# Kernel optimization log

Measured on AMD Instinct MI355X. Metric: run time of the kernel, lower is better.

Reference implementation:

```python
import jax, jax.numpy as jnp
import numpy as np

H = 1024


def setup_inputs() -> dict:
    key = jax.random.key(0)
    ks = jax.random.split(key, 7)
    x = jax.random.normal(ks[0], (8, 2048, H), dtype=jnp.float32)
    s = 1.0 / np.sqrt(H)
    Wq = jax.random.normal(ks[1], (H, H), dtype=jnp.float32) * s
    bq = jnp.zeros((H,), dtype=jnp.float32)
    Wk = jax.random.normal(ks[2], (H, H), dtype=jnp.float32) * s
    bk = jnp.zeros((H,), dtype=jnp.float32)
    Wv = jax.random.normal(ks[3], (H, H), dtype=jnp.float32) * s
    bv = jnp.zeros((H,), dtype=jnp.float32)
    return {"x": x, "Wq": Wq, "bq": bq, "Wk": Wk, "bk": bk, "Wv": Wv, "bv": bv}


def reference(x, Wq, bq, Wk, bk, Wv, bv):
    # q,k,v: [B,S,H]
    q = jnp.einsum('bsh,hd->bsd', x, Wq) + bq
    k = jnp.einsum('bsh,hd->bsd', x, Wk) + bk
    v = jnp.einsum('bsh,hd->bsd', x, Wv) + bv
    scale = 1.0 / jnp.sqrt(jnp.asarray(x.shape[-1], dtype=x.dtype))
    scores = jnp.einsum('bqd,bkd->bqk', q, k) * scale  # [B,S,S]
    attn = jax.nn.softmax(scores, axis=-1)
    return jnp.einsum('bqk,bkd->bqd', attn, v)
```

## Files before the change

### kernel.cpp

```cpp
#include <hip/hip_runtime.h>

typedef _Float16 half8  __attribute__((ext_vector_type(8)));
typedef _Float16 half4v __attribute__((ext_vector_type(4)));
typedef float    floatx4 __attribute__((ext_vector_type(4)));

#define GLD_LDS16(g, l)                                                        \
  __builtin_amdgcn_global_load_lds(                                            \
      (const __attribute__((address_space(1))) void*)(g),                      \
      (__attribute__((address_space(3))) void*)(l), 16, 0, 0)

template <int EPI>
__global__ __launch_bounds__(256) void gemm_bt(
    const _Float16* __restrict__ A, const _Float16* __restrict__ B,
    void* __restrict__ Cv, void* __restrict__ Cv2, int lda, int ldb, int ldc,
    int kdim, long long sAz, long long sBz, long long sCz,
    const float* __restrict__ b0, const float* __restrict__ b1,
    const float* __restrict__ b2, float* __restrict__ rowsum, float scale) {
  __shared__ _Float16 sA[128 * 64];
  __shared__ _Float16 sB[128 * 64];

  const int bid = blockIdx.x;
  int z, m0, n0;
  if (EPI == 0) {
    const int xcd = bid & 7, j = bid >> 3;
    z = j >> 7;
    m0 = (xcd * 16 + ((j >> 3) & 15)) * 128;
    n0 = (j & 7) * 128;
  } else if (EPI == 2) {
    z = bid & 7;
    const int j = bid >> 3;
    m0 = (j >> 4) * 128;
    n0 = (j & 15) * 128;
  } else {
    z = bid & 7;
    const int j = bid >> 3;
    m0 = (j >> 3) * 128;
    n0 = (j & 7) * 128;
  }

  A += (size_t)z * sAz;
  B += (size_t)z * sBz;

  const int tid = threadIdx.x;
  const int wid = tid >> 6;
  const int lane = tid & 63;

  const int wm = (wid & 1) * 64;
  const int wn = (wid >> 1) * 64;
  const int lr = lane & 15;
  const int lk = lane >> 4;

  floatx4 acc[4][4];
#pragma unroll
  for (int i = 0; i < 4; ++i)
#pragma unroll
    for (int j = 0; j < 4; ++j)
#pragma unroll
      for (int r = 0; r < 4; ++r) acc[i][j][r] = 0.f;

  const _Float16* gA[4];
  const _Float16* gB[4];
  int ub[4];
#pragma unroll
  for (int j = 0; j < 4; ++j) {
    const int s = j * 256 + wid * 64 + lane;
    const int row = s >> 3;
    const int kc = (s & 7) ^ (row & 7);
    gA[j] = A + (size_t)(m0 + row) * lda + kc * 8;
    gB[j] = B + (size_t)(n0 + row) * ldb + kc * 8;
    ub[j] = (j * 256 + wid * 64) * 8;
  }

  for (int k0 = 0; k0 < kdim; k0 += 64) {
#pragma unroll
    for (int j = 0; j < 4; ++j) {
      GLD_LDS16(gA[j], &sA[ub[j]]);
      GLD_LDS16(gB[j], &sB[ub[j]]);
      gA[j] += 64;
      gB[j] += 64;
    }
    __syncthreads();

#pragma unroll
    for (int ks = 0; ks < 2; ++ks) {
      half8 af[4], bf[4];
#pragma unroll
      for (int t = 0; t < 4; ++t) {
        const int kcl = ks * 4 + lk;
        const int ra = wm + t * 16 + lr;
        af[t] = *(const half8*)&sA[(ra * 8 + (kcl ^ (ra & 7))) * 8];
        const int rb = wn + t * 16 + lr;
        bf[t] = *(const half8*)&sB[(rb * 8 + (kcl ^ (rb & 7))) * 8];
      }
#pragma unroll
      for (int mt = 0; mt < 4; ++mt)
#pragma unroll
        for (int nt = 0; nt < 4; ++nt)
          acc[mt][nt] = __builtin_amdgcn_mfma_f32_16x16x32_f16(
              af[mt], bf[nt], acc[mt][nt], 0, 0, 0);
    }
    __syncthreads();
  }

  if (EPI == 0) {
    const float* bias = (z == 0) ? b0 : ((z == 1) ? b1 : b2);
#pragma unroll
    for (int mt = 0; mt < 4; ++mt) {
#pragma unroll
      for (int nt = 0; nt < 4; ++nt) {
#pragma unroll
        for (int r = 0; r < 4; ++r) {
          const int gm = m0 + wm + mt * 16 + lk * 4 + r;
          const int gn = n0 + wn + nt * 16 + lr;
          const float v = acc[mt][nt][r] + bias[gn];
          if (z < 2) {
            ((_Float16*)Cv)[(size_t)z * 16777216 + (size_t)gm * 1024 + gn] =
                (_Float16)v;
          } else {
            const int b = gm >> 11, sseq = gm & 2047;
            ((_Float16*)Cv2)[(size_t)b * 2097152 + (size_t)gn * 2048 + sseq] =
                (_Float16)v;
          }
        }
      }
    }
  } else if (EPI == 2) {
    const float c1 = scale * 1.44269504f;
    const float c0 = -5.77078016f;
    _Float16* Sout = (_Float16*)Cv + (size_t)z * sCz;
    float* rs = rowsum + z * 2048;
#pragma unroll
    for (int mt = 0; mt < 4; ++mt) {
#pragma unroll
      for (int r = 0; r < 4; ++r) {
        const int gm = m0 + wm + mt * 16 + lk * 4 + r;
        float part = 0.f;
#pragma unroll
        for (int nt = 0; nt < 4; ++nt) {
          const int gn = n0 + wn + nt * 16 + lr;
          const float p = exp2f(fmaf(acc[mt][nt][r], c1, c0));
          const _Float16 ph = (_Float16)p;
          Sout[(size_t)gm * ldc + gn] = ph;
          part += (float)ph;
        }
#pragma unroll
        for (int o = 1; o < 16; o <<= 1) part += __shfl_xor(part, o);
        if (lr == 0) atomicAdd(&rs[gm], part);
      }
    }
  } else {
    float* O = (float*)Cv + (size_t)z * sCz;
    const float* rs = rowsum + z * 2048;
#pragma unroll
    for (int mt = 0; mt < 4; ++mt) {
#pragma unroll
      for (int r = 0; r < 4; ++r) {
        const int gm = m0 + wm + mt * 16 + lk * 4 + r;
        const float inv = 1.0f / rs[gm];
#pragma unroll
        for (int nt = 0; nt < 4; ++nt) {
          const int gn = n0 + wn + nt * 16 + lr;
          O[(size_t)gm * ldc + gn] = acc[mt][nt][r] * inv;
        }
      }
    }
  }
}

__global__ __launch_bounds__(256) void prep(
    const float* __restrict__ x, _Float16* __restrict__ xb,
    const float* __restrict__ W0, const float* __restrict__ W1,
    const float* __restrict__ W2, _Float16* __restrict__ Wt) {
  const int bid = blockIdx.x;
  const int tid = threadIdx.x;
  if (bid < 16384) {
    const int i = bid * 256 + tid;
    const float4 v = ((const float4*)x)[i];
    half4v h;
    h[0] = (_Float16)v.x;
    h[1] = (_Float16)v.y;
    h[2] = (_Float16)v.z;
    h[3] = (_Float16)v.w;
    ((half4v*)xb)[i] = h;
    return;
  }
  __shared__ float tile[32][33];
  const int q = bid - 16384;
  const int bz = q >> 10;
  const int t = q & 1023;
  const int d0 = (t & 31) * 32, h0 = (t >> 5) * 32;
  const float* W = bz == 0 ? W0 : (bz == 1 ? W1 : W2);
  _Float16* T = Wt + (size_t)bz * 1048576;
  const int tx = tid & 31, ty = tid >> 5;
#pragma unroll
  for (int i = 0; i < 4; ++i)
    tile[ty + i * 8][tx] = W[(size_t)(h0 + ty + i * 8) * 1024 + d0 + tx];
  __syncthreads();
#pragma unroll
  for (int i = 0; i < 4; ++i)
    T[(size_t)(d0 + ty + i * 8) * 1024 + h0 + tx] =
        (_Float16)tile[tx][ty + i * 8];
}

extern "C" void kernel_launch(void* const* d_in, const int* in_sizes, int n_in,
                              void* d_out, int out_size, void* d_ws,
                              size_t ws_size, hipStream_t stream) {
  const float* x = (const float*)d_in[0];
  const float* Wq = (const float*)d_in[1];
  const float* bq = (const float*)d_in[2];
  const float* Wk = (const float*)d_in[3];
  const float* bk = (const float*)d_in[4];
  const float* Wv = (const float*)d_in[5];
  const float* bv = (const float*)d_in[6];
  float* out = (float*)d_out;

  char* w = (char*)d_ws;
  _Float16* xb = (_Float16*)(w);
  _Float16* Wt = (_Float16*)(w + 33554432);
  _Float16* QK = (_Float16*)(w + 39845888);
  _Float16* Vt = (_Float16*)(w + 106954752);
  _Float16* S  = (_Float16*)(w + 140509184);
  float* rowsum = (float*)(w);

  prep<<<19456, 256, 0, stream>>>(x, xb, Wq, Wk, Wv, Wt);
  gemm_bt<0><<<3072, 256, 0, stream>>>(
      xb, Wt, QK, Vt, 1024, 1024, 1024, 1024, 0LL, 1048576LL, 0LL, bq, bk, bv,
      nullptr, 1.f);
  hipMemsetAsync(rowsum, 0, 8 * 2048 * sizeof(float), stream);
  gemm_bt<2><<<2048, 256, 0, stream>>>(
      QK, QK + 16777216, S, nullptr, 1024, 1024, 2048, 1024, 2097152LL,
      2097152LL, 4194304LL, nullptr, nullptr, nullptr, rowsum, 0.03125f);
  gemm_bt<3><<<1024, 256, 0, stream>>>(
      S, Vt, out, nullptr, 2048, 2048, 1024, 2048, 4194304LL, 2097152LL,
      2097152LL, nullptr, nullptr, nullptr, rowsum, 1.f);

  (void)in_sizes;
  (void)n_in;
  (void)out_size;
  (void)ws_size;
}
```

Baseline: 479.7 us.

## Use 256x256 tiles with 8 waves and double-buffered LDS ping-pong pipeline

Grows the GEMM tile from 128x128 to 256x256 and the block from 256 to 512 threads. The K loop becomes double-buffered in 128 KB of LDS, with global-to-LDS prefetch of the next K tile interleaved between MFMA phases using explicit vmcnt waits, barriers and setprio. The aim is to hide global load latency, raise data reuse per tile and improve MFMA utilisation. In exchange it uses more registers and LDS, and grid sizes drop (256 blocks for the final GEMM), which may underfill the 256 CUs.

```diff
diff --git a/kernel.cpp b/kernel.cpp
--- a/kernel.cpp
+++ b/kernel.cpp
@@ -9,33 +9,133 @@
       (const __attribute__((address_space(1))) void*)(g),                      \
       (__attribute__((address_space(3))) void*)(l), 16, 0, 0)
 
+#define SBAR() __builtin_amdgcn_s_barrier()
+#define WAITVM2() asm volatile("s_waitcnt vmcnt(2)" ::: "memory")
+#define WAITVM0() asm volatile("s_waitcnt vmcnt(0)" ::: "memory")
+#define SCHED0() __builtin_amdgcn_sched_barrier(0)
+
+
+#define STG_A(c, ht, ko)                                                       \
+  do {                                                                         \
+    GLD_LDS16(A0 + (size_t)(ht) * lda128 + (ko),                               \
+              &lds[(c) * 32768 + ((ht) * 1024 + wid * 128) * 8]);              \
+    GLD_LDS16(A1 + (size_t)(ht) * lda128 + (ko),                               \
+              &lds[(c) * 32768 + ((ht) * 1024 + wid * 128 + 64) * 8]);         \
+  } while (0)
+#define STG_B(c, ht, ko)                                                       \
+  do {                                                                         \
+    GLD_LDS16(B0 + (size_t)(ht) * ldb128 + (ko),                               \
+              &lds[(c) * 32768 + 16384 + ((ht) * 1024 + wid * 128) * 8]);      \
+    GLD_LDS16(B1 + (size_t)(ht) * ldb128 + (ko),                               \
+              &lds[(c) * 32768 + 16384 + ((ht) * 1024 + wid * 128 + 64) * 8]); \
+  } while (0)
+
+#define RDA(dst, c, mt, ks)                                                    \
+  do {                                                                         \
+    const int ra_ = wm + (mt) * 16 + lr;                                       \
+    dst = *(const half8*)&lds[(c) * 32768 +                                    \
+                              (ra_ * 8 + (((ks) * 4 + lk) ^ (ra_ & 7))) * 8];  \
+  } while (0)
+#define RDB(dst, c, nt, ks)                                                    \
+  do {                                                                         \
+    const int rb_ = wn + (nt) * 16 + lr;                                       \
+    dst = *(const half8*)&lds[(c) * 32768 + 16384 +                            \
+                              (rb_ * 8 + (((ks) * 4 + lk) ^ (rb_ & 7))) * 8];  \
+  } while (0)
+
+#define MM4x2(MB, NB, BF)                                                      \
+  do {                                                                         \
+    _Pragma("unroll") for (int mt_ = 0; mt_ < 4; ++mt_)                        \
+        _Pragma("unroll") for (int n_ = 0; n_ < 2; ++n_)                       \
+            _Pragma("unroll") for (int ks_ = 0; ks_ < 2; ++ks_)                \
+                acc[(MB) + mt_][(NB) + n_] =                                   \
+        __builtin_amdgcn_mfma_f32_16x16x32_f16(                                \
+            af[mt_][ks_], BF[n_][ks_], acc[(MB) + mt_][(NB) + n_], 0, 0, 0);   \
+  } while (0)
+
+#define KBLOCK(CUR, KT)                                                        \
+  do {                                                                         \
+    const int ko_ = ((KT) + 1) << 6;                                           \
+    const bool pf_ = ((KT) + 1 < NT);                                          \
+       \
+    if (pf_) {                                                                 \
+      STG_A(1 - (CUR), 0, ko_);                                                \
+      WAITVM2();                                                               \
+    } else {                                                                   \
+      WAITVM0();                                                               \
+    }                                                                          \
+    SBAR();                                                                    \
+    SCHED0();                                                                  \
+    RDA(af[0][0], CUR, 0, 0); RDA(af[0][1], CUR, 0, 1);                        \
+    RDA(af[1][0], CUR, 1, 0); RDA(af[1][1], CUR, 1, 1);                        \
+    RDA(af[2][0], CUR, 2, 0); RDA(af[2][1], CUR, 2, 1);                        \
+    RDA(af[3][0], CUR, 3, 0); RDA(af[3][1], CUR, 3, 1);                        \
+    RDB(bf0[0][0], CUR, 0, 0); RDB(bf0[0][1], CUR, 0, 1);                      \
+    RDB(bf0[1][0], CUR, 1, 0); RDB(bf0[1][1], CUR, 1, 1);                      \
+    SBAR();                                                                    \
+    SCHED0();                                                                  \
+    __builtin_amdgcn_s_setprio(1);                                             \
+    MM4x2(0, 0, bf0);                                                          \
+    __builtin_amdgcn_s_setprio(0);                                             \
+    SBAR();                                                                    \
+                \
+    RDB(bf1[0][0], CUR, 2, 0); RDB(bf1[0][1], CUR, 2, 1);                      \
+    RDB(bf1[1][0], CUR, 3, 0); RDB(bf1[1][1], CUR, 3, 1);                      \
+    if (pf_) STG_B(1 - (CUR), 0, ko_);                                         \
+    SBAR();                                                                    \
+    SCHED0();                                                                  \
+    __builtin_amdgcn_s_setprio(1);                                             \
+    MM4x2(0, 2, bf1);                                                          \
+    __builtin_amdgcn_s_setprio(0);                                             \
+    SBAR();                                                                    \
+                        \
+    RDA(af[0][0], CUR, 4, 0); RDA(af[0][1], CUR, 4, 1);                        \
+    RDA(af[1][0], CUR, 5, 0); RDA(af[1][1], CUR, 5, 1);                        \
+    RDA(af[2][0], CUR, 6, 0); RDA(af[2][1], CUR, 6, 1);                        \
+    RDA(af[3][0], CUR, 7, 0); RDA(af[3][1], CUR, 7, 1);                        \
+    if (pf_) STG_A(1 - (CUR), 1, ko_);                                         \
+    SBAR();                                                                    \
+    SCHED0();                                                                  \
+    __builtin_amdgcn_s_setprio(1);                                             \
+    MM4x2(4, 2, bf1);                                                          \
+    __builtin_amdgcn_s_setprio(0);                                             \
+    SBAR();                                                                    \
+             \
+    if (pf_) STG_B(1 - (CUR), 1, ko_);                                         \
+    SBAR();                                                                    \
+    SCHED0();                                                                  \
+    __builtin_amdgcn_s_setprio(1);                                             \
+    MM4x2(4, 0, bf0);                                                          \
+    __builtin_amdgcn_s_setprio(0);                                             \
+    SBAR();                                                                    \
+  } while (0)
+
 template <int EPI>
-__global__ __launch_bounds__(256) void gemm_bt(
+__global__ __launch_bounds__(512, 2) void gemm_bt(
     const _Float16* __restrict__ A, const _Float16* __restrict__ B,
     void* __restrict__ Cv, void* __restrict__ Cv2, int lda, int ldb, int ldc,
     int kdim, long long sAz, long long sBz, long long sCz,
     const float* __restrict__ b0, const float* __restrict__ b1,
     const float* __restrict__ b2, float* __restrict__ rowsum, float scale) {
-  __shared__ _Float16 sA[128 * 64];
-  __shared__ _Float16 sB[128 * 64];
+  __shared__ _Float16 lds[65536];
 
   const int bid = blockIdx.x;
   int z, m0, n0;
   if (EPI == 0) {
     const int xcd = bid & 7, j = bid >> 3;
-    z = j >> 7;
-    m0 = (xcd * 16 + ((j >> 3) & 15)) * 128;
-    n0 = (j & 7) * 128;
+    z = j >> 5;
+    m0 = (xcd * 8 + ((j >> 2) & 7)) * 256;
+    n0 = (j & 3) * 256;
   } else if (EPI == 2) {
     z = bid & 7;
     const int j = bid >> 3;
-    m0 = (j >> 4) * 128;
-    n0 = (j & 15) * 128;
+    m0 = (j >> 3) * 256;
+    n0 = (j & 7) * 256;
   } else {
     z = bid & 7;
     const int j = bid >> 3;
-    m0 = (j >> 3) * 128;
-    n0 = (j & 7) * 128;
+    m0 = (j >> 2) * 256;
+    n0 = (j & 3) * 256;
   }
 
   A += (size_t)z * sAz;
@@ -44,68 +144,50 @@
   const int tid = threadIdx.x;
   const int wid = tid >> 6;
   const int lane = tid & 63;
-
-  const int wm = (wid & 1) * 64;
+  const int wm = (wid & 1) * 128;
   const int wn = (wid >> 1) * 64;
   const int lr = lane & 15;
   const int lk = lane >> 4;
 
-  floatx4 acc[4][4];
-#pragma unroll
-  for (int i = 0; i < 4; ++i)
+  floatx4 acc[8][4];
+#pragma unroll
+  for (int i = 0; i < 8; ++i)
 #pragma unroll
     for (int j = 0; j < 4; ++j)
 #pragma unroll
       for (int r = 0; r < 4; ++r) acc[i][j][r] = 0.f;
 
-  const _Float16* gA[4];
-  const _Float16* gB[4];
-  int ub[4];
-#pragma unroll
-  for (int j = 0; j < 4; ++j) {
-    const int s = j * 256 + wid * 64 + lane;
-    const int row = s >> 3;
-    const int kc = (s & 7) ^ (row & 7);
-    gA[j] = A + (size_t)(m0 + row) * lda + kc * 8;
-    gB[j] = B + (size_t)(n0 + row) * ldb + kc * 8;
-    ub[j] = (j * 256 + wid * 64) * 8;
-  }
-
-  for (int k0 = 0; k0 < kdim; k0 += 64) {
-#pragma unroll
-    for (int j = 0; j < 4; ++j) {
-      GLD_LDS16(gA[j], &sA[ub[j]]);
-      GLD_LDS16(gB[j], &sB[ub[j]]);
-      gA[j] += 64;
-      gB[j] += 64;
-    }
-    __syncthreads();
-
-#pragma unroll
-    for (int ks = 0; ks < 2; ++ks) {
-      half8 af[4], bf[4];
-#pragma unroll
-      for (int t = 0; t < 4; ++t) {
-        const int kcl = ks * 4 + lk;
-        const int ra = wm + t * 16 + lr;
-        af[t] = *(const half8*)&sA[(ra * 8 + (kcl ^ (ra & 7))) * 8];
-        const int rb = wn + t * 16 + lr;
-        bf[t] = *(const half8*)&sB[(rb * 8 + (kcl ^ (rb & 7))) * 8];
-      }
-#pragma unroll
-      for (int mt = 0; mt < 4; ++mt)
-#pragma unroll
-        for (int nt = 0; nt < 4; ++nt)
-          acc[mt][nt] = __builtin_amdgcn_mfma_f32_16x16x32_f16(
-              af[mt], bf[nt], acc[mt][nt], 0, 0, 0);
-    }
-    __syncthreads();
+  const int s0 = wid * 128 + lane;
+  const int s1 = s0 + 64;
+  const int r0 = s0 >> 3, c0 = (s0 & 7) ^ (r0 & 7);
+  const int r1 = s1 >> 3, c1 = (s1 & 7) ^ (r1 & 7);
+  const _Float16* A0 = A + (size_t)(m0 + r0) * lda + c0 * 8;
+  const _Float16* A1 = A + (size_t)(m0 + r1) * lda + c1 * 8;
+  const _Float16* B0 = B + (size_t)(n0 + r0) * ldb + c0 * 8;
+  const _Float16* B1 = B + (size_t)(n0 + r1) * ldb + c1 * 8;
+  const size_t lda128 = (size_t)lda * 128;
+  const size_t ldb128 = (size_t)ldb * 128;
+
+  const int NT = kdim >> 6;
+
+  STG_A(0, 0, 0);
+  STG_B(0, 0, 0);
+  STG_A(0, 1, 0);
+  STG_B(0, 1, 0);
+  WAITVM0();
+  SBAR();
+
+  half8 af[4][2], bf0[2][2], bf1[2][2];
+
+  for (int kt = 0; kt < NT; kt += 2) {
+    KBLOCK(0, kt);
+    KBLOCK(1, kt + 1);
   }
 
   if (EPI == 0) {
     const float* bias = (z == 0) ? b0 : ((z == 1) ? b1 : b2);
 #pragma unroll
-    for (int mt = 0; mt < 4; ++mt) {
+    for (int mt = 0; mt < 8; ++mt) {
 #pragma unroll
       for (int nt = 0; nt < 4; ++nt) {
 #pragma unroll
@@ -126,11 +208,11 @@
     }
   } else if (EPI == 2) {
     const float c1 = scale * 1.44269504f;
-    const float c0 = -5.77078016f;
+    const float c0e = -5.77078016f;
     _Float16* Sout = (_Float16*)Cv + (size_t)z * sCz;
     float* rs = rowsum + z * 2048;
 #pragma unroll
-    for (int mt = 0; mt < 4; ++mt) {
+    for (int mt = 0; mt < 8; ++mt) {
 #pragma unroll
       for (int r = 0; r < 4; ++r) {
         const int gm = m0 + wm + mt * 16 + lk * 4 + r;
@@ -138,7 +220,7 @@
 #pragma unroll
         for (int nt = 0; nt < 4; ++nt) {
           const int gn = n0 + wn + nt * 16 + lr;
-          const float p = exp2f(fmaf(acc[mt][nt][r], c1, c0));
+          const float p = exp2f(fmaf(acc[mt][nt][r], c1, c0e));
           const _Float16 ph = (_Float16)p;
           Sout[(size_t)gm * ldc + gn] = ph;
           part += (float)ph;
@@ -152,7 +234,7 @@
     float* O = (float*)Cv + (size_t)z * sCz;
     const float* rs = rowsum + z * 2048;
 #pragma unroll
-    for (int mt = 0; mt < 4; ++mt) {
+    for (int mt = 0; mt < 8; ++mt) {
 #pragma unroll
       for (int r = 0; r < 4; ++r) {
         const int gm = m0 + wm + mt * 16 + lk * 4 + r;
@@ -219,20 +301,21 @@
   _Float16* Wt = (_Float16*)(w + 33554432);
   _Float16* QK = (_Float16*)(w + 39845888);
   _Float16* Vt = (_Float16*)(w + 106954752);
-  _Float16* S  = (_Float16*)(w + 140509184);
+  _Float16* S = (_Float16*)(w + 140509184);
   float* rowsum = (float*)(w);
 
   prep<<<19456, 256, 0, stream>>>(x, xb, Wq, Wk, Wv, Wt);
-  gemm_bt<0><<<3072, 256, 0, stream>>>(
-      xb, Wt, QK, Vt, 1024, 1024, 1024, 1024, 0LL, 1048576LL, 0LL, bq, bk, bv,
-      nullptr, 1.f);
+  gemm_bt<0><<<768, 512, 0, stream>>>(xb, Wt, QK, Vt, 1024, 1024, 1024, 1024,
+                                      0LL, 1048576LL, 0LL, bq, bk, bv, nullptr,
+                                      1.f);
   hipMemsetAsync(rowsum, 0, 8 * 2048 * sizeof(float), stream);
-  gemm_bt<2><<<2048, 256, 0, stream>>>(
-      QK, QK + 16777216, S, nullptr, 1024, 1024, 2048, 1024, 2097152LL,
-      2097152LL, 4194304LL, nullptr, nullptr, nullptr, rowsum, 0.03125f);
-  gemm_bt<3><<<1024, 256, 0, stream>>>(
-      S, Vt, out, nullptr, 2048, 2048, 1024, 2048, 4194304LL, 2097152LL,
-      2097152LL, nullptr, nullptr, nullptr, rowsum, 1.f);
+  gemm_bt<2><<<512, 512, 0, stream>>>(QK, QK + 16777216, S, nullptr, 1024,
+                                      1024, 2048, 1024, 2097152LL, 2097152LL,
+                                      4194304LL, nullptr, nullptr, nullptr,
+                                      rowsum, 0.03125f);
+  gemm_bt<3><<<256, 512, 0, stream>>>(S, Vt, out, nullptr, 2048, 2048, 1024,
+                                      2048, 4194304LL, 2097152LL, 2097152LL,
+                                      nullptr, nullptr, nullptr, rowsum, 1.f);
 
   (void)in_sizes;
   (void)n_in;
```

Measured after the change: 411.7 us. 1.17x faster.

## Double-buffer GEMM LDS with 256x128 tiles and 512-thread blocks

Applied to the files above, without the earlier changes.

Restructures the shared GEMM kernel to use 512-thread blocks computing 256x128 output tiles with a 32-wide K step. LDS is double-buffered, so the next K slice is prefetched with global_load_lds while the current one feeds the MFMAs, using explicit vmcnt waits, raw barriers and setprio around the MFMA block. This is meant to hide global load latency behind compute and halve the number of blocks. In exchange each K step does less work per barrier, and the smaller swizzle width may change LDS bank behaviour.

```diff
diff --git a/kernel.cpp b/kernel.cpp
--- a/kernel.cpp
+++ b/kernel.cpp
@@ -9,32 +9,83 @@
       (const __attribute__((address_space(1))) void*)(g),                      \
       (__attribute__((address_space(3))) void*)(l), 16, 0, 0)
 
+#define SBAR() __builtin_amdgcn_s_barrier()
+#define WAITVM3() asm volatile("s_waitcnt vmcnt(3)" ::: "memory")
+#define WAITVM0() asm volatile("s_waitcnt vmcnt(0)" ::: "memory")
+#define SCHED0() __builtin_amdgcn_sched_barrier(0)
+
+
+#define STG(c, ko)                                                             \
+  do {                                                                         \
+    GLD_LDS16(gA0 + (ko), &lds[(c) * 12288 + tid * 8]);                        \
+    GLD_LDS16(gA1 + (ko), &lds[(c) * 12288 + (512 + tid) * 8]);               \
+    GLD_LDS16(gB0 + (ko), &lds[(c) * 12288 + 8192 + tid * 8]);                \
+  } while (0)
+
+#define RDA(dst, c, mt)                                                        \
+  do {                                                                         \
+    const int ra_ = wm + (mt) * 16 + lr;                                       \
+    dst = *(const half8*)&lds[(c) * 12288 +                                    \
+                              (ra_ * 4 + (lk ^ (ra_ & 3))) * 8];               \
+  } while (0)
+#define RDB(dst, c, nt)                                                        \
+  do {                                                                         \
+    const int rb_ = wn + (nt) * 16 + lr;                                       \
+    dst = *(const half8*)&lds[(c) * 12288 + 8192 +                             \
+                              (rb_ * 4 + (lk ^ (rb_ & 3))) * 8];               \
+  } while (0)
+
+#define KBLOCK(CUR, KT)                                                        \
+  do {                                                                         \
+    const int ko_ = ((KT) + 1) << 5;                                           \
+    const bool pf_ = ((KT) + 1 < NT);                                          \
+    if (pf_) {                                                                 \
+      STG(1 - (CUR), ko_);                                                     \
+      WAITVM3();                                                               \
+    } else {                                                                   \
+      WAITVM0();                                                               \
+    }                                                                          \
+    SBAR();                                                                    \
+    SCHED0();                                                                  \
+    half8 af[4], bf[4];                                                        \
+    RDA(af[0], CUR, 0); RDA(af[1], CUR, 1);                                    \
+    RDA(af[2], CUR, 2); RDA(af[3], CUR, 3);                                    \
+    RDB(bf[0], CUR, 0); RDB(bf[1], CUR, 1);                                    \
+    RDB(bf[2], CUR, 2); RDB(bf[3], CUR, 3);                                    \
+    __builtin_amdgcn_s_setprio(1);                                             \
+    _Pragma("unroll") for (int mt_ = 0; mt_ < 4; ++mt_)                        \
+        _Pragma("unroll") for (int nt_ = 0; nt_ < 4; ++nt_)                    \
+            acc[mt_][nt_] = __builtin_amdgcn_mfma_f32_16x16x32_f16(            \
+                af[mt_], bf[nt_], acc[mt_][nt_], 0, 0, 0);                     \
+    __builtin_amdgcn_s_setprio(0);                                             \
+    SBAR();                                                                    \
+  } while (0)
+
 template <int EPI>
-__global__ __launch_bounds__(256) void gemm_bt(
+__global__ __launch_bounds__(512, 4) void gemm_bt(
     const _Float16* __restrict__ A, const _Float16* __restrict__ B,
     void* __restrict__ Cv, void* __restrict__ Cv2, int lda, int ldb, int ldc,
     int kdim, long long sAz, long long sBz, long long sCz,
     const float* __restrict__ b0, const float* __restrict__ b1,
     const float* __restrict__ b2, float* __restrict__ rowsum, float scale) {
-  __shared__ _Float16 sA[128 * 64];
-  __shared__ _Float16 sB[128 * 64];
+  __shared__ _Float16 lds[24576];
 
   const int bid = blockIdx.x;
   int z, m0, n0;
   if (EPI == 0) {
     const int xcd = bid & 7, j = bid >> 3;
-    z = j >> 7;
-    m0 = (xcd * 16 + ((j >> 3) & 15)) * 128;
+    z = j >> 6;
+    m0 = (xcd * 8 + ((j >> 3) & 7)) * 256;
     n0 = (j & 7) * 128;
   } else if (EPI == 2) {
     z = bid & 7;
     const int j = bid >> 3;
-    m0 = (j >> 4) * 128;
+    m0 = (j >> 4) * 256;
     n0 = (j & 15) * 128;
   } else {
     z = bid & 7;
     const int j = bid >> 3;
-    m0 = (j >> 3) * 128;
+    m0 = (j >> 3) * 256;
     n0 = (j & 7) * 128;
   }
 
@@ -44,9 +95,8 @@
   const int tid = threadIdx.x;
   const int wid = tid >> 6;
   const int lane = tid & 63;
-
-  const int wm = (wid & 1) * 64;
-  const int wn = (wid >> 1) * 64;
+  const int wm = (wid >> 1) * 64;
+  const int wn = (wid & 1) * 64;
   const int lr = lane & 15;
   const int lk = lane >> 4;
 
@@ -58,48 +108,25 @@
 #pragma unroll
       for (int r = 0; r < 4; ++r) acc[i][j][r] = 0.f;
 
-  const _Float16* gA[4];
-  const _Float16* gB[4];
-  int ub[4];
-#pragma unroll
-  for (int j = 0; j < 4; ++j) {
-    const int s = j * 256 + wid * 64 + lane;
-    const int row = s >> 3;
-    const int kc = (s & 7) ^ (row & 7);
-    gA[j] = A + (size_t)(m0 + row) * lda + kc * 8;
-    gB[j] = B + (size_t)(n0 + row) * ldb + kc * 8;
-    ub[j] = (j * 256 + wid * 64) * 8;
-  }
-
-  for (int k0 = 0; k0 < kdim; k0 += 64) {
-#pragma unroll
-    for (int j = 0; j < 4; ++j) {
-      GLD_LDS16(gA[j], &sA[ub[j]]);
-      GLD_LDS16(gB[j], &sB[ub[j]]);
-      gA[j] += 64;
-      gB[j] += 64;
-    }
-    __syncthreads();
-
-#pragma unroll
-    for (int ks = 0; ks < 2; ++ks) {
-      half8 af[4], bf[4];
-#pragma unroll
-      for (int t = 0; t < 4; ++t) {
-        const int kcl = ks * 4 + lk;
-        const int ra = wm + t * 16 + lr;
-        af[t] = *(const half8*)&sA[(ra * 8 + (kcl ^ (ra & 7))) * 8];
-        const int rb = wn + t * 16 + lr;
-        bf[t] = *(const half8*)&sB[(rb * 8 + (kcl ^ (rb & 7))) * 8];
-      }
-#pragma unroll
-      for (int mt = 0; mt < 4; ++mt)
-#pragma unroll
-        for (int nt = 0; nt < 4; ++nt)
-          acc[mt][nt] = __builtin_amdgcn_mfma_f32_16x16x32_f16(
-              af[mt], bf[nt], acc[mt][nt], 0, 0, 0);
-    }
-    __syncthreads();
+  {
+  }
+  const int sa0 = tid, sa1 = tid + 512, sb0 = tid;
+  const int ra0 = sa0 >> 2, ca0 = (sa0 & 3) ^ (ra0 & 3);
+  const int ra1 = sa1 >> 2, ca1 = (sa1 & 3) ^ (ra1 & 3);
+  const int rb0 = sb0 >> 2, cb0 = (sb0 & 3) ^ (rb0 & 3);
+  const _Float16* gA0 = A + (size_t)(m0 + ra0) * lda + ca0 * 8;
+  const _Float16* gA1 = A + (size_t)(m0 + ra1) * lda + ca1 * 8;
+  const _Float16* gB0 = B + (size_t)(n0 + rb0) * ldb + cb0 * 8;
+
+  const int NT = kdim >> 5;
+
+  STG(0, 0);
+  WAITVM0();
+  SBAR();
+
+  for (int kt = 0; kt < NT; kt += 2) {
+    KBLOCK(0, kt);
+    KBLOCK(1, kt + 1);
   }
 
   if (EPI == 0) {
@@ -126,7 +153,7 @@
     }
   } else if (EPI == 2) {
     const float c1 = scale * 1.44269504f;
-    const float c0 = -5.77078016f;
+    const float c0e = -5.77078016f;
     _Float16* Sout = (_Float16*)Cv + (size_t)z * sCz;
     float* rs = rowsum + z * 2048;
 #pragma unroll
@@ -138,7 +165,7 @@
 #pragma unroll
         for (int nt = 0; nt < 4; ++nt) {
           const int gn = n0 + wn + nt * 16 + lr;
-          const float p = exp2f(fmaf(acc[mt][nt][r], c1, c0));
+          const float p = exp2f(fmaf(acc[mt][nt][r], c1, c0e));
           const _Float16 ph = (_Float16)p;
           Sout[(size_t)gm * ldc + gn] = ph;
           part += (float)ph;
@@ -219,20 +246,21 @@
   _Float16* Wt = (_Float16*)(w + 33554432);
   _Float16* QK = (_Float16*)(w + 39845888);
   _Float16* Vt = (_Float16*)(w + 106954752);
-  _Float16* S  = (_Float16*)(w + 140509184);
+  _Float16* S = (_Float16*)(w + 140509184);
   float* rowsum = (float*)(w);
 
   prep<<<19456, 256, 0, stream>>>(x, xb, Wq, Wk, Wv, Wt);
-  gemm_bt<0><<<3072, 256, 0, stream>>>(
-      xb, Wt, QK, Vt, 1024, 1024, 1024, 1024, 0LL, 1048576LL, 0LL, bq, bk, bv,
-      nullptr, 1.f);
+  gemm_bt<0><<<1536, 512, 0, stream>>>(xb, Wt, QK, Vt, 1024, 1024, 1024, 1024,
+                                       0LL, 1048576LL, 0LL, bq, bk, bv,
+                                       nullptr, 1.f);
   hipMemsetAsync(rowsum, 0, 8 * 2048 * sizeof(float), stream);
-  gemm_bt<2><<<2048, 256, 0, stream>>>(
-      QK, QK + 16777216, S, nullptr, 1024, 1024, 2048, 1024, 2097152LL,
-      2097152LL, 4194304LL, nullptr, nullptr, nullptr, rowsum, 0.03125f);
-  gemm_bt<3><<<1024, 256, 0, stream>>>(
-      S, Vt, out, nullptr, 2048, 2048, 1024, 2048, 4194304LL, 2097152LL,
-      2097152LL, nullptr, nullptr, nullptr, rowsum, 1.f);
+  gemm_bt<2><<<1024, 512, 0, stream>>>(QK, QK + 16777216, S, nullptr, 1024,
+                                       1024, 2048, 1024, 2097152LL, 2097152LL,
+                                       4194304LL, nullptr, nullptr, nullptr,
+                                       rowsum, 0.03125f);
+  gemm_bt<3><<<512, 512, 0, stream>>>(S, Vt, out, nullptr, 2048, 2048, 1024,
+                                      2048, 4194304LL, 2097152LL, 2097152LL,
+                                      nullptr, nullptr, nullptr, rowsum, 1.f);
 
   (void)in_sizes;
   (void)n_in;
```

Measured after the change: 428.5 us. 1.12x faster.
